# Optimization experiments

Measured on AMD Instinct MI355X. Metric: run time of the kernel, lower is better.

## Reference

```python
import jax, jax.numpy as jnp
import numpy as np

B, T, H, N_IN, N_OUT = 256, 1024, 512, 64, 64


def setup_inputs() -> dict:
    key = jax.random.key(0)
    k_x, k_w, k_win, k_wout = jax.random.split(key, 4)
    # nn.Linear(in, out, bias=False) weight has shape [out, in]
    X = jax.random.normal(k_x, (B, T, N_IN), dtype=jnp.float32)
    h0 = jnp.zeros((B, H), dtype=jnp.float32)
    W = jax.random.normal(k_w, (H, H), dtype=jnp.float32) / np.sqrt(H)
    W_in = jax.random.normal(k_win, (H, N_IN), dtype=jnp.float32) / np.sqrt(N_IN)
    W_out = jax.random.normal(k_wout, (N_OUT, H), dtype=jnp.float32) / np.sqrt(H)
    return {"X": X, "h0": h0, "W": W, "W_in": W_in, "W_out": W_out}


def reference(X, h0, W, W_in, W_out):
    # Precompute input projections for all timesteps in one big GEMM:
    # inp[b, t, h] = X[b, t, :] @ W_in.T  (same math as per-step W_in(x_t))
    inp = jnp.einsum("bti,hi->tbh", X, W_in)  # [T, B, H]

    def step(h, inp_t):
        h_next = jnp.tanh(h) @ W.T + inp_t  # [B, H]
        return h_next, h_next

    _, hidden = jax.lax.scan(step, h0, inp)  # hidden: [T, B, H]
    hidden = jnp.transpose(hidden, (1, 0, 2))  # [B, T, H]
    out = jnp.einsum("bth,oh->bto", hidden, W_out)  # [B, T, n_out]
    return out, hidden
```

## Files before the change

kernel.cpp:

```cpp
#include <hip/hip_runtime.h>
#include <stdint.h>

#define B_    256
#define T_    1024
#define H_    512
#define NIN_  64
#define NOUT_ 64

#define NW     8
#define BBLK   4
#define KB_TOT 18
#define KB_REG 14
#define KB_LDS 4
#define HROW   592

typedef __attribute__((ext_vector_type(8))) short bf16x8;
typedef __attribute__((ext_vector_type(4))) float f32x4;

__device__ __forceinline__ short f2bf(float f) {
  uint32_t u = __float_as_uint(f);
  uint32_t r = (u + 0x7FFFu + ((u >> 16) & 1u)) >> 16;
  return (short)(r & 0xFFFFu);
}

__device__ __forceinline__ bf16x8 pack8(float4 lo, float4 hi) {
  bf16x8 s;
  s[0] = f2bf(lo.x); s[1] = f2bf(lo.y); s[2] = f2bf(lo.z); s[3] = f2bf(lo.w);
  s[4] = f2bf(hi.x); s[5] = f2bf(hi.y); s[6] = f2bf(hi.z); s[7] = f2bf(hi.w);
  return s;
}

__device__ __forceinline__ float fast_tanh(float x) {
  float e = __expf(2.0f * x);
  return 1.0f - __fdividef(2.0f, e + 1.0f);
}

__global__ __launch_bounds__(NW * 64, 2) void rnn_scan(
    const float* __restrict__ X, const float* __restrict__ h0,
    const float* __restrict__ W, const float* __restrict__ Win,
    float* __restrict__ hid)
{
  __shared__ __align__(16) short wlds[KB_LDS][H_][32];
  __shared__ __align__(16) short hbuf[2][BBLK][HROW];

  const int tid  = threadIdx.x;
  const int lane = tid & 63;
  const int w    = tid >> 6;
  const int g    = lane >> 4;
  const int m    = lane & 15;
  const int b0   = blockIdx.x * BBLK;

  bf16x8 Wf[KB_REG][4];
#pragma unroll
  for (int kb = 0; kb < KB_REG; ++kb) {
#pragma unroll
    for (int jt = 0; jt < 4; ++jt) {
      const int j = 64 * w + 16 * jt + m;
      const float4* p = reinterpret_cast<const float4*>(W + (size_t)j * H_ + 32 * kb + 8 * g);
      Wf[kb][jt] = pack8(p[0], p[1]);
    }
  }

#pragma unroll
  for (int i = 0; i < 16; ++i) {
    const int c   = tid + 512 * i;
    const int kbp = c >> 11;
    const int col = (c >> 2) & 511;
    const int q   = (c & 3) * 8;
    const float* src = (kbp < 2) ? (W   + (size_t)col * H_   + 32 * (KB_REG + kbp) + q)
                                 : (Win + (size_t)col * NIN_ + 32 * (kbp - 2)      + q);
    const float4* p = reinterpret_cast<const float4*>(src);
    *reinterpret_cast<bf16x8*>(&wlds[kbp][col][q]) = pack8(p[0], p[1]);
  }

  for (int e = tid; e < BBLK * H_; e += NW * 64) {
    const int r = e >> 9, k = e & (H_ - 1);
    hbuf[0][r][k] = f2bf(fast_tanh(h0[(size_t)(b0 + r) * H_ + k]));
  }
  if (tid < BBLK * NIN_) {
    const int r = tid >> 6, kk = tid & 63;
    hbuf[0][r][H_ + kk] = f2bf(X[((size_t)(b0 + r) * T_ + 0) * NIN_ + kk]);
  }
  __syncthreads();

  for (int t = 0; t < T_; ++t) {
    const int cur = t & 1, nxt = cur ^ 1;
    const short* hrow = &hbuf[cur][m & 3][0];

    float xpf = 0.f;
    {
      const int tn = (t + 1 < T_) ? (t + 1) : t;
      if (tid < BBLK * NIN_)
        xpf = X[((size_t)(b0 + (tid >> 6)) * T_ + tn) * NIN_ + (tid & 63)];
    }

    f32x4 acc[4];
    {
      const bf16x8 a = *reinterpret_cast<const bf16x8*>(hrow + 32 * KB_REG + 8 * g);
#pragma unroll
      for (int jt = 0; jt < 4; ++jt) {
        const bf16x8 b = *reinterpret_cast<const bf16x8*>(&wlds[0][64 * w + 16 * jt + m][8 * g]);
        const f32x4 zero = {0.f, 0.f, 0.f, 0.f};
        acc[jt] = __builtin_amdgcn_mfma_f32_16x16x32_bf16(a, b, zero, 0, 0, 0);
      }
    }
#pragma unroll
    for (int kb = KB_REG + 1; kb < KB_TOT; ++kb) {
      const bf16x8 a = *reinterpret_cast<const bf16x8*>(hrow + 32 * kb + 8 * g);
#pragma unroll
      for (int jt = 0; jt < 4; ++jt) {
        const bf16x8 b = *reinterpret_cast<const bf16x8*>(&wlds[kb - KB_REG][64 * w + 16 * jt + m][8 * g]);
        acc[jt] = __builtin_amdgcn_mfma_f32_16x16x32_bf16(a, b, acc[jt], 0, 0, 0);
      }
    }
#pragma unroll
    for (int kb = 0; kb < KB_REG; ++kb) {
      const bf16x8 a = *reinterpret_cast<const bf16x8*>(hrow + 32 * kb + 8 * g);
#pragma unroll
      for (int jt = 0; jt < 4; ++jt)
        acc[jt] = __builtin_amdgcn_mfma_f32_16x16x32_bf16(a, Wf[kb][jt], acc[jt], 0, 0, 0);
    }

#pragma unroll
    for (int r = 0; r < 4; ++r) {
      float v = acc[0][r];
      v = (g == 1) ? acc[1][r] : v;
      v = (g == 2) ? acc[2][r] : v;
      v = (g == 3) ? acc[3][r] : v;
      hid[((size_t)(b0 + r) * T_ + t) * H_ + 64 * w + lane] = v;
      hbuf[nxt][r][64 * w + lane] = f2bf(fast_tanh(v));
    }
    if (tid < BBLK * NIN_)
      hbuf[nxt][tid >> 6][H_ + (tid & 63)] = f2bf(xpf);

    asm volatile("s_waitcnt lgkmcnt(0)" ::: "memory");
    __builtin_amdgcn_s_barrier();
  }
}

#define OP_BLOCKS 1024
#define OP_WAVES  8
__global__ __launch_bounds__(OP_WAVES * 64, 2) void out_proj(
    const float* __restrict__ hid, const float* __restrict__ Wout,
    float* __restrict__ out)
{
  __shared__ __align__(16) short ws[16][NOUT_][32];

  const int tid  = threadIdx.x;
  const int lane = tid & 63;
  const int w    = tid >> 6;
  const int g    = lane >> 4;
  const int m    = lane & 15;

#pragma unroll
  for (int i = 0; i < 8; ++i) {
    const int c   = tid + OP_WAVES * 64 * i;
    const int kb  = c >> 8;
    const int col = (c >> 2) & 63;
    const int q   = (c & 3) * 8;
    const float4* p = reinterpret_cast<const float4*>(Wout + (size_t)col * H_ + 32 * kb + q);
    *reinterpret_cast<bf16x8*>(&ws[kb][col][q]) = pack8(p[0], p[1]);
  }
  __syncthreads();

  const int wave_id = blockIdx.x * OP_WAVES + w;
  const int NWAVES  = OP_BLOCKS * OP_WAVES;
  const int NTILES  = (B_ * T_) / 16;

  for (int tile = wave_id; tile < NTILES; tile += NWAVES) {
    const size_t row0 = (size_t)tile * 16;
    f32x4 acc[4];
    {
      const float4* p = reinterpret_cast<const float4*>(hid + (row0 + m) * H_ + 8 * g);
      const bf16x8 a = pack8(p[0], p[1]);
#pragma unroll
      for (int jt = 0; jt < 4; ++jt) {
        const bf16x8 b = *reinterpret_cast<const bf16x8*>(&ws[0][16 * jt + m][8 * g]);
        const f32x4 zero = {0.f, 0.f, 0.f, 0.f};
        acc[jt] = __builtin_amdgcn_mfma_f32_16x16x32_bf16(a, b, zero, 0, 0, 0);
      }
    }
#pragma unroll
    for (int kb = 1; kb < 16; ++kb) {
      const float4* p = reinterpret_cast<const float4*>(hid + (row0 + m) * H_ + 32 * kb + 8 * g);
      const bf16x8 a = pack8(p[0], p[1]);
#pragma unroll
      for (int jt = 0; jt < 4; ++jt) {
        const bf16x8 b = *reinterpret_cast<const bf16x8*>(&ws[kb][16 * jt + m][8 * g]);
        acc[jt] = __builtin_amdgcn_mfma_f32_16x16x32_bf16(a, b, acc[jt], 0, 0, 0);
      }
    }
#pragma unroll
    for (int jt = 0; jt < 4; ++jt) {
#pragma unroll
      for (int r = 0; r < 4; ++r)
        out[(row0 + 4 * g + r) * NOUT_ + 16 * jt + m] = acc[jt][r];
    }
  }
}

extern "C" void kernel_launch(void* const* d_in, const int* in_sizes, int n_in,
                              void* d_out, int out_size, void* d_ws, size_t ws_size,
                              hipStream_t stream) {
  const float* X    = (const float*)d_in[0];
  const float* h0   = (const float*)d_in[1];
  const float* W    = (const float*)d_in[2];
  const float* Win  = (const float*)d_in[3];
  const float* Wout = (const float*)d_in[4];

  float* out = (float*)d_out;
  float* hid = (float*)d_out + (size_t)B_ * T_ * NOUT_;

  rnn_scan<<<dim3(B_ / BBLK), dim3(NW * 64), 0, stream>>>(X, h0, W, Win, hid);
  out_proj<<<dim3(OP_BLOCKS), dim3(OP_WAVES * 64), 0, stream>>>(hid, Wout, out);
}
```

Measured before the change: 2.583 ms.

## Precompute input projection in separate kernel and shrink scan to four waves

Adds an xproj kernel that computes X·W_in^T into the hidden buffer ahead of the scan. The scan then reads that buffer and adds it in fp32 instead of folding X into the recurrent MFMA K dimension. The scan block drops from 8 to 4 waves, each owning 128 output columns, with about 100 W fragments held in registers and the rest in LDS. The per-step input values are prefetched one step ahead. This cuts the per-step MFMA count and barrier participants, at the cost of heavy register pressure, one wave per SIMD, and an extra global read and write pass over the hidden buffer.

Result: slower. 3.493 ms (+35.2%).

```diff
diff --git a/kernel.cpp b/kernel.cpp
--- a/kernel.cpp
+++ b/kernel.cpp
@@ -7,12 +7,12 @@
 #define NIN_  64
 #define NOUT_ 64
 
-#define NW     8
 #define BBLK   4
-#define KB_TOT 18
-#define KB_REG 14
-#define KB_LDS 4
-#define HROW   592
+#define SC_NW  4
+#define KB_N   16
+#define RU     100
+#define LU     28
+#define HROW   528
 
 typedef __attribute__((ext_vector_type(8))) short bf16x8;
 typedef __attribute__((ext_vector_type(4))) float f32x4;
@@ -35,12 +35,60 @@
   return 1.0f - __fdividef(2.0f, e + 1.0f);
 }
 
-__global__ __launch_bounds__(NW * 64, 2) void rnn_scan(
-    const float* __restrict__ X, const float* __restrict__ h0,
-    const float* __restrict__ W, const float* __restrict__ Win,
+#define XP_BLOCKS 512
+__global__ __launch_bounds__(512, 2) void xproj(
+    const float* __restrict__ X, const float* __restrict__ Win,
+    float* __restrict__ inp)
+{
+  const int tid  = threadIdx.x;
+  const int lane = tid & 63;
+  const int w    = tid >> 6;
+  const int g    = lane >> 4;
+  const int m    = lane & 15;
+
+  bf16x8 Bf[2][4];
+#pragma unroll
+  for (int kb = 0; kb < 2; ++kb)
+#pragma unroll
+    for (int jt = 0; jt < 4; ++jt) {
+      const int j = 64 * w + 16 * jt + m;
+      const float4* p = reinterpret_cast<const float4*>(Win + (size_t)j * NIN_ + 32 * kb + 8 * g);
+      Bf[kb][jt] = pack8(p[0], p[1]);
+    }
+
+  const int NTILES = (B_ * T_) / 16;
+  const f32x4 zero = {0.f, 0.f, 0.f, 0.f};
+
+  for (int tile = blockIdx.x; tile < NTILES; tile += XP_BLOCKS) {
+    const size_t row0 = (size_t)tile * 16;
+    f32x4 acc[4];
+    {
+      const float4* p = reinterpret_cast<const float4*>(X + (row0 + m) * NIN_ + 8 * g);
+      const bf16x8 a = pack8(p[0], p[1]);
+#pragma unroll
+      for (int jt = 0; jt < 4; ++jt)
+        acc[jt] = __builtin_amdgcn_mfma_f32_16x16x32_bf16(a, Bf[0][jt], zero, 0, 0, 0);
+    }
+    {
+      const float4* p = reinterpret_cast<const float4*>(X + (row0 + m) * NIN_ + 32 + 8 * g);
+      const bf16x8 a = pack8(p[0], p[1]);
+#pragma unroll
+      for (int jt = 0; jt < 4; ++jt)
+        acc[jt] = __builtin_amdgcn_mfma_f32_16x16x32_bf16(a, Bf[1][jt], acc[jt], 0, 0, 0);
+    }
+#pragma unroll
+    for (int jt = 0; jt < 4; ++jt)
+#pragma unroll
+      for (int r = 0; r < 4; ++r)
+        inp[(row0 + 4 * g + r) * H_ + 64 * w + 16 * jt + m] = acc[jt][r];
+  }
+}
+
+__global__ __launch_bounds__(SC_NW * 64, 1) void rnn_scan(
+    const float* __restrict__ h0, const float* __restrict__ W,
     float* __restrict__ hid)
 {
-  __shared__ __align__(16) short wlds[KB_LDS][H_][32];
+  __shared__ __align__(16) short wlds[LU][64][32];
   __shared__ __align__(16) short hbuf[2][BBLK][HROW];
 
   const int tid  = threadIdx.x;
@@ -50,91 +98,115 @@
   const int m    = lane & 15;
   const int b0   = blockIdx.x * BBLK;
 
-  bf16x8 Wf[KB_REG][4];
-#pragma unroll
-  for (int kb = 0; kb < KB_REG; ++kb) {
-#pragma unroll
-    for (int jt = 0; jt < 4; ++jt) {
-      const int j = 64 * w + 16 * jt + m;
+  bf16x8 Wf[RU];
+#pragma unroll
+  for (int kb = 0; kb < 12; ++kb)
+#pragma unroll
+    for (int jt = 0; jt < 8; ++jt) {
+      const int j = 128 * w + 16 * jt + m;
       const float4* p = reinterpret_cast<const float4*>(W + (size_t)j * H_ + 32 * kb + 8 * g);
-      Wf[kb][jt] = pack8(p[0], p[1]);
-    }
-  }
-
-#pragma unroll
-  for (int i = 0; i < 16; ++i) {
-    const int c   = tid + 512 * i;
-    const int kbp = c >> 11;
-    const int col = (c >> 2) & 511;
-    const int q   = (c & 3) * 8;
-    const float* src = (kbp < 2) ? (W   + (size_t)col * H_   + 32 * (KB_REG + kbp) + q)
-                                 : (Win + (size_t)col * NIN_ + 32 * (kbp - 2)      + q);
-    const float4* p = reinterpret_cast<const float4*>(src);
-    *reinterpret_cast<bf16x8*>(&wlds[kbp][col][q]) = pack8(p[0], p[1]);
-  }
-
-  for (int e = tid; e < BBLK * H_; e += NW * 64) {
+      Wf[kb * 8 + jt] = pack8(p[0], p[1]);
+    }
+#pragma unroll
+  for (int jt = 0; jt < 4; ++jt) {
+    const int j = 128 * w + 16 * jt + m;
+    const float4* p = reinterpret_cast<const float4*>(W + (size_t)j * H_ + 32 * 12 + 8 * g);
+    Wf[96 + jt] = pack8(p[0], p[1]);
+  }
+
+#pragma unroll
+  for (int i = 0; i < LU; ++i) {
+    const int c  = tid + 256 * i;
+    const int u  = c >> 8;
+    const int s  = c & 255;
+    const int wm = s >> 2;
+    const int gq = s & 3;
+    int kb, jt;
+    if (u < 4) { kb = 12; jt = 4 + u; } else { kb = 13 + ((u - 4) >> 3); jt = (u - 4) & 7; }
+    const int j = 128 * (wm >> 4) + 16 * jt + (wm & 15);
+    const float4* p = reinterpret_cast<const float4*>(W + (size_t)j * H_ + 32 * kb + 8 * gq);
+    *reinterpret_cast<bf16x8*>(&wlds[u][wm][gq * 8]) = pack8(p[0], p[1]);
+  }
+
+  for (int e = tid; e < BBLK * H_; e += SC_NW * 64) {
     const int r = e >> 9, k = e & (H_ - 1);
     hbuf[0][r][k] = f2bf(fast_tanh(h0[(size_t)(b0 + r) * H_ + k]));
   }
-  if (tid < BBLK * NIN_) {
-    const int r = tid >> 6, kk = tid & 63;
-    hbuf[0][r][H_ + kk] = f2bf(X[((size_t)(b0 + r) * T_ + 0) * NIN_ + kk]);
-  }
+
+  float inp_cur[2][4];
+#pragma unroll
+  for (int jtp = 0; jtp < 2; ++jtp) {
+    const int col = 128 * w + 16 * (g + 4 * jtp) + m;
+#pragma unroll
+    for (int r = 0; r < 4; ++r)
+      inp_cur[jtp][r] = hid[((size_t)(b0 + r) * T_ + 0) * H_ + col];
+  }
+
   __syncthreads();
 
+  const f32x4 zero = {0.f, 0.f, 0.f, 0.f};
+  const int arow = m & 3;
+
+#pragma clang loop unroll(disable)
   for (int t = 0; t < T_; ++t) {
     const int cur = t & 1, nxt = cur ^ 1;
-    const short* hrow = &hbuf[cur][m & 3][0];
-
-    float xpf = 0.f;
-    {
-      const int tn = (t + 1 < T_) ? (t + 1) : t;
-      if (tid < BBLK * NIN_)
-        xpf = X[((size_t)(b0 + (tid >> 6)) * T_ + tn) * NIN_ + (tid & 63)];
-    }
-
-    f32x4 acc[4];
-    {
-      const bf16x8 a = *reinterpret_cast<const bf16x8*>(hrow + 32 * KB_REG + 8 * g);
-#pragma unroll
-      for (int jt = 0; jt < 4; ++jt) {
-        const bf16x8 b = *reinterpret_cast<const bf16x8*>(&wlds[0][64 * w + 16 * jt + m][8 * g]);
-        const f32x4 zero = {0.f, 0.f, 0.f, 0.f};
-        acc[jt] = __builtin_amdgcn_mfma_f32_16x16x32_bf16(a, b, zero, 0, 0, 0);
-      }
-    }
-#pragma unroll
-    for (int kb = KB_REG + 1; kb < KB_TOT; ++kb) {
-      const bf16x8 a = *reinterpret_cast<const bf16x8*>(hrow + 32 * kb + 8 * g);
-#pragma unroll
-      for (int jt = 0; jt < 4; ++jt) {
-        const bf16x8 b = *reinterpret_cast<const bf16x8*>(&wlds[kb - KB_REG][64 * w + 16 * jt + m][8 * g]);
+
+    float inp_nxt[2][4];
+    if (t + 1 < T_) {
+#pragma unroll
+      for (int jtp = 0; jtp < 2; ++jtp) {
+        const int col = 128 * w + 16 * (g + 4 * jtp) + m;
+#pragma unroll
+        for (int r = 0; r < 4; ++r)
+          inp_nxt[jtp][r] = hid[((size_t)(b0 + r) * T_ + (t + 1)) * H_ + col];
+      }
+    }
+
+    f32x4 acc[8];
+#pragma unroll
+    for (int jt = 0; jt < 8; ++jt) acc[jt] = zero;
+
+#pragma unroll
+    for (int kb = 0; kb < KB_N; ++kb) {
+      const bf16x8 a = *reinterpret_cast<const bf16x8*>(&hbuf[cur][arow][32 * kb + 8 * g]);
+#pragma unroll
+      for (int jt = 0; jt < 8; ++jt) {
+        bf16x8 b;
+        if (kb < 12)
+          b = Wf[kb * 8 + jt];
+        else if (kb == 12 && jt < 4)
+          b = Wf[96 + jt];
+        else {
+          const int u = (kb == 12) ? (jt - 4) : (4 + (kb - 13) * 8 + jt);
+          b = *reinterpret_cast<const bf16x8*>(&wlds[u][w * 16 + m][g * 8]);
+        }
         acc[jt] = __builtin_amdgcn_mfma_f32_16x16x32_bf16(a, b, acc[jt], 0, 0, 0);
       }
     }
-#pragma unroll
-    for (int kb = 0; kb < KB_REG; ++kb) {
-      const bf16x8 a = *reinterpret_cast<const bf16x8*>(hrow + 32 * kb + 8 * g);
-#pragma unroll
-      for (int jt = 0; jt < 4; ++jt)
-        acc[jt] = __builtin_amdgcn_mfma_f32_16x16x32_bf16(a, Wf[kb][jt], acc[jt], 0, 0, 0);
-    }
-
-#pragma unroll
-    for (int r = 0; r < 4; ++r) {
-      float v = acc[0][r];
-      v = (g == 1) ? acc[1][r] : v;
-      v = (g == 2) ? acc[2][r] : v;
-      v = (g == 3) ? acc[3][r] : v;
-      hid[((size_t)(b0 + r) * T_ + t) * H_ + 64 * w + lane] = v;
-      hbuf[nxt][r][64 * w + lane] = f2bf(fast_tanh(v));
-    }
-    if (tid < BBLK * NIN_)
-      hbuf[nxt][tid >> 6][H_ + (tid & 63)] = f2bf(xpf);
+
+#pragma unroll
+    for (int jtp = 0; jtp < 2; ++jtp) {
+      const int col = 128 * w + 16 * (g + 4 * jtp) + m;
+#pragma unroll
+      for (int r = 0; r < 4; ++r) {
+        float v;
+        if (jtp == 0)
+          v = (g == 0) ? acc[0][r] : (g == 1) ? acc[1][r] : (g == 2) ? acc[2][r] : acc[3][r];
+        else
+          v = (g == 0) ? acc[4][r] : (g == 1) ? acc[5][r] : (g == 2) ? acc[6][r] : acc[7][r];
+        v += inp_cur[jtp][r];
+        hid[((size_t)(b0 + r) * T_ + t) * H_ + col] = v;
+        hbuf[nxt][r][col] = f2bf(fast_tanh(v));
+      }
+    }
+#pragma unroll
+    for (int jtp = 0; jtp < 2; ++jtp)
+#pragma unroll
+      for (int r = 0; r < 4; ++r) inp_cur[jtp][r] = inp_nxt[jtp][r];
 
     asm volatile("s_waitcnt lgkmcnt(0)" ::: "memory");
     __builtin_amdgcn_s_barrier();
+    asm volatile("" ::: "memory");
   }
 }
 
@@ -173,10 +245,10 @@
     {
       const float4* p = reinterpret_cast<const float4*>(hid + (row0 + m) * H_ + 8 * g);
       const bf16x8 a = pack8(p[0], p[1]);
+      const f32x4 zero = {0.f, 0.f, 0.f, 0.f};
 #pragma unroll
       for (int jt = 0; jt < 4; ++jt) {
         const bf16x8 b = *reinterpret_cast<const bf16x8*>(&ws[0][16 * jt + m][8 * g]);
-        const f32x4 zero = {0.f, 0.f, 0.f, 0.f};
         acc[jt] = __builtin_amdgcn_mfma_f32_16x16x32_bf16(a, b, zero, 0, 0, 0);
       }
     }
@@ -191,11 +263,10 @@
       }
     }
 #pragma unroll
-    for (int jt = 0; jt < 4; ++jt) {
+    for (int jt = 0; jt < 4; ++jt)
 #pragma unroll
       for (int r = 0; r < 4; ++r)
         out[(row0 + 4 * g + r) * NOUT_ + 16 * jt + m] = acc[jt][r];
-    }
   }
 }
 
@@ -211,6 +282,7 @@
   float* out = (float*)d_out;
   float* hid = (float*)d_out + (size_t)B_ * T_ * NOUT_;
 
-  rnn_scan<<<dim3(B_ / BBLK), dim3(NW * 64), 0, stream>>>(X, h0, W, Win, hid);
+  xproj<<<dim3(XP_BLOCKS), dim3(512), 0, stream>>>(X, Win, hid);
+  rnn_scan<<<dim3(B_ / BBLK), dim3(SC_NW * 64), 0, stream>>>(h0, W, hid);
   out_proj<<<dim3(OP_BLOCKS), dim3(OP_WAVES * 64), 0, stream>>>(hid, Wout, out);
 }
```
